# Kernel optimization log

Hardware: AMD Instinct MI355X
Metric: run time of the kernel (lower is better)

Reference implementation:

```python
import jax, jax.numpy as jnp
import numpy as np

B, H, S, D = 2, 16, 2048, 64

def setup_inputs() -> dict:
    key = jax.random.key(0)
    kq, kk, kv = jax.random.split(key, 3)
    q = jax.random.normal(kq, (B, H, S, D), dtype=jnp.float32)
    k = jax.random.normal(kk, (B, H, S, D), dtype=jnp.float32)
    v = jax.random.normal(kv, (B, H, S, D), dtype=jnp.float32)
    # causal mask: True where position j > i (future tokens are masked)
    mask = jnp.triu(jnp.ones((S, S), dtype=bool), k=1)[None, None, :, :]
    return {"q": q, "k": k, "v": v, "mask": mask}

def reference(q, k, v, mask) -> jnp.ndarray:
    # scaled dot-product attention with additive -1e4 mask bias
    scale = 1.0 / jnp.sqrt(jnp.asarray(q.shape[-1], q.dtype))
    scores = jnp.einsum('bhqd,bhkd->bhqk', q, k) * scale  # [B,H,S,S]
    scores = scores + mask.astype(scores.dtype) * jnp.asarray(-10000.0, scores.dtype)
    probs = jax.nn.softmax(scores, axis=-1)
    # dropout is identity in eval mode
    return jnp.einsum('bhqk,bhkd->bhqd', probs, v)
```

## Files before the change

kernel.cpp:

```cpp
#include <hip/hip_runtime.h>

typedef __bf16 bf16_t;
typedef bf16_t bf16x8 __attribute__((ext_vector_type(8)));
typedef bf16_t bf16x4 __attribute__((ext_vector_type(4)));
typedef float  floatx4 __attribute__((ext_vector_type(4)));

constexpr int Sq = 2048, Dq = 64;
constexpr int BQ = 64, BK = 64;
constexpr int NQT = Sq / BQ;
constexpr int STR = 72;
constexpr float SCALE_LOG2E = 0.125f * 1.44269504088896340736f;

__global__ __launch_bounds__(256, 2) void flash_attn_kernel(
    const float* __restrict__ Q, const float* __restrict__ K,
    const float* __restrict__ V, float* __restrict__ O)
{
    __shared__ bf16_t QPs[BQ][STR];
    __shared__ bf16_t Ks[BK][STR];
    __shared__ bf16_t VTs[Dq][STR];

    const int tid  = threadIdx.x;
    const int wave = tid >> 6;
    const int lane = tid & 63;
    const int quad = lane >> 4;
    const int l16  = lane & 15;

    const int id = blockIdx.x;
    const int bh = (id & 7) + ((id >> 7) << 3);
    const int pr = (id >> 3) & 15;
    const long base = (long)bh * Sq * Dq;

    const int r0 = tid >> 4;
    const int c4 = (tid & 15) * 4;
    const int h  = lane >> 3;
    const int jw = wave * 16;

    for (int half = 0; half < 2; ++half) {
        const int qt = half ? (NQT - 1 - pr) : pr;

        __syncthreads();
        #pragma unroll
        for (int p = 0; p < 4; ++p) {
            const int row = p * 16 + r0;
            const float4 qv = *(const float4*)&Q[base + (long)(qt * BQ + row) * Dq + c4];
            bf16x4 w;
            w[0] = (bf16_t)(qv.x * SCALE_LOG2E); w[1] = (bf16_t)(qv.y * SCALE_LOG2E);
            w[2] = (bf16_t)(qv.z * SCALE_LOG2E); w[3] = (bf16_t)(qv.w * SCALE_LOG2E);
            *(bf16x4*)&QPs[row][c4] = w;
        }
        __syncthreads();

        bf16x8 aq0, aq1;
        {
            const int qrow = wave * 16 + l16;
            aq0 = *(const bf16x8*)&QPs[qrow][quad * 8];
            aq1 = *(const bf16x8*)&QPs[qrow][32 + quad * 8];
        }

        float l_lane = 0.f;
        floatx4 o_acc[4];
        #pragma unroll
        for (int i = 0; i < 4; ++i) o_acc[i] = floatx4{0.f, 0.f, 0.f, 0.f};

        float4 kf[4];
        float  vf[4][4];
        #pragma unroll
        for (int p = 0; p < 4; ++p) {
            kf[p] = *(const float4*)&K[base + (long)(p * 16 + r0) * Dq + c4];
            const int j0 = jw + 4 * ((p + h) & 3);
            #pragma unroll
            for (int r = 0; r < 4; ++r)
                vf[p][r] = V[base + (long)(j0 + r) * Dq + lane];
        }

        for (int kt = 0; kt <= qt; ++kt) {
            __syncthreads();

            #pragma unroll
            for (int p = 0; p < 4; ++p) {
                bf16x4 w;
                w[0] = (bf16_t)kf[p].x; w[1] = (bf16_t)kf[p].y;
                w[2] = (bf16_t)kf[p].z; w[3] = (bf16_t)kf[p].w;
                *(bf16x4*)&Ks[p * 16 + r0][c4] = w;
                bf16x4 vw;
                vw[0] = (bf16_t)vf[p][0]; vw[1] = (bf16_t)vf[p][1];
                vw[2] = (bf16_t)vf[p][2]; vw[3] = (bf16_t)vf[p][3];
                *(bf16x4*)&VTs[lane][jw + 4 * ((p + h) & 3)] = vw;
            }
            __syncthreads();

            {
                const int kn = (kt < qt) ? (kt + 1) : qt;
                const long kb = base + (long)kn * BK * Dq;
                #pragma unroll
                for (int p = 0; p < 4; ++p) {
                    kf[p] = *(const float4*)&K[kb + (long)(p * 16 + r0) * Dq + c4];
                    const int j0 = jw + 4 * ((p + h) & 3);
                    #pragma unroll
                    for (int r = 0; r < 4; ++r)
                        vf[p][r] = V[kb + (long)(j0 + r) * Dq + lane];
                }
            }

            floatx4 acc[4];
            #pragma unroll
            for (int t = 0; t < 4; ++t) {
                acc[t] = floatx4{0.f, 0.f, 0.f, 0.f};
                const int krow = t * 16 + l16;
                bf16x8 ak0 = *(const bf16x8*)&Ks[krow][quad * 8];
                bf16x8 ak1 = *(const bf16x8*)&Ks[krow][32 + quad * 8];
                acc[t] = __builtin_amdgcn_mfma_f32_16x16x32_bf16(ak0, aq0, acc[t], 0, 0, 0);
                acc[t] = __builtin_amdgcn_mfma_f32_16x16x32_bf16(ak1, aq1, acc[t], 0, 0, 0);
            }

            if (kt == qt) {
                const int qr = wave * 16 + l16;
                #pragma unroll
                for (int t = 0; t < 4; ++t) {
                    #pragma unroll
                    for (int i = 0; i < 4; ++i) {
                        if (t * 16 + quad * 4 + i > qr) acc[t][i] = -1e30f;
                    }
                }
            }

            float l_add = 0.f;
            #pragma unroll
            for (int t = 0; t < 4; ++t) {
                #pragma unroll
                for (int i = 0; i < 4; ++i) {
                    acc[t][i] = __builtin_amdgcn_exp2f(acc[t][i]);
                    l_add += acc[t][i];
                }
            }
            l_lane += l_add;

            #pragma unroll
            for (int t = 0; t < 4; ++t) {
                bf16x4 pk;
                pk[0] = (bf16_t)acc[t][0]; pk[1] = (bf16_t)acc[t][1];
                pk[2] = (bf16_t)acc[t][2]; pk[3] = (bf16_t)acc[t][3];
                *(bf16x4*)&QPs[wave * 16 + l16][t * 16 + quad * 4] = pk;
            }

            bf16x8 ap0 = *(const bf16x8*)&QPs[wave * 16 + l16][quad * 8];
            bf16x8 ap1 = *(const bf16x8*)&QPs[wave * 16 + l16][32 + quad * 8];
            #pragma unroll
            for (int dt = 0; dt < 4; ++dt) {
                const int dcol = dt * 16 + l16;
                bf16x8 bv0 = *(const bf16x8*)&VTs[dcol][quad * 8];
                bf16x8 bv1 = *(const bf16x8*)&VTs[dcol][32 + quad * 8];
                o_acc[dt] = __builtin_amdgcn_mfma_f32_16x16x32_bf16(ap0, bv0, o_acc[dt], 0, 0, 0);
                o_acc[dt] = __builtin_amdgcn_mfma_f32_16x16x32_bf16(ap1, bv1, o_acc[dt], 0, 0, 0);
            }
        }

        float lsum = l_lane;
        lsum += __shfl_xor(lsum, 16);
        lsum += __shfl_xor(lsum, 32);
        #pragma unroll
        for (int i = 0; i < 4; ++i) {
            const float inv_l = 1.f / __shfl(lsum, quad * 4 + i, 16);
            const long row = (long)qt * BQ + wave * 16 + quad * 4 + i;
            #pragma unroll
            for (int dt = 0; dt < 4; ++dt) {
                O[base + row * Dq + dt * 16 + l16] = o_acc[dt][i] * inv_l;
            }
        }
    }
}

extern "C" void kernel_launch(void* const* d_in, const int* in_sizes, int n_in,
                              void* d_out, int out_size, void* d_ws, size_t ws_size,
                              hipStream_t stream)
{
    const float* q = (const float*)d_in[0];
    const float* k = (const float*)d_in[1];
    const float* v = (const float*)d_in[2];
    float* out = (float*)d_out;
    flash_attn_kernel<<<dim3(512, 1, 1), dim3(256, 1, 1), 0, stream>>>(q, k, v, out);
}
```

Measured before the change: 128.2 us.

## Double-buffer K/V tiles in LDS and raise wave priority around MFMAs

K and V tiles go into two LDS buffers, so the next tile is written after the PV matmul and only one barrier per iteration is needed instead of two. Global loads for the next tile are issued before the QK MFMAs. s_setprio raises wave priority during the MFMA blocks, and the exp-sum reduction is reassociated into a tree. The cost is about twice the LDS for K/V and more live registers, which may affect occupancy.

```diff
diff --git a/kernel.cpp b/kernel.cpp
--- a/kernel.cpp
+++ b/kernel.cpp
@@ -16,8 +16,8 @@
     const float* __restrict__ V, float* __restrict__ O)
 {
     __shared__ bf16_t QPs[BQ][STR];
-    __shared__ bf16_t Ks[BK][STR];
-    __shared__ bf16_t VTs[Dq][STR];
+    __shared__ bf16_t Ks[2][BK][STR];
+    __shared__ bf16_t VTs[2][Dq][STR];
 
     const int tid  = threadIdx.x;
     const int wave = tid >> 6;
@@ -62,36 +62,32 @@
         #pragma unroll
         for (int i = 0; i < 4; ++i) o_acc[i] = floatx4{0.f, 0.f, 0.f, 0.f};
 
-        float4 kf[4];
-        float  vf[4][4];
-        #pragma unroll
-        for (int p = 0; p < 4; ++p) {
-            kf[p] = *(const float4*)&K[base + (long)(p * 16 + r0) * Dq + c4];
-            const int j0 = jw + 4 * ((p + h) & 3);
+        {
             #pragma unroll
-            for (int r = 0; r < 4; ++r)
-                vf[p][r] = V[base + (long)(j0 + r) * Dq + lane];
+            for (int p = 0; p < 4; ++p) {
+                const float4 kv = *(const float4*)&K[base + (long)(p * 16 + r0) * Dq + c4];
+                bf16x4 w;
+                w[0] = (bf16_t)kv.x; w[1] = (bf16_t)kv.y;
+                w[2] = (bf16_t)kv.z; w[3] = (bf16_t)kv.w;
+                *(bf16x4*)&Ks[0][p * 16 + r0][c4] = w;
+                const int j0 = jw + 4 * ((p + h) & 3);
+                bf16x4 vw;
+                #pragma unroll
+                for (int r = 0; r < 4; ++r)
+                    vw[r] = (bf16_t)V[base + (long)(j0 + r) * Dq + lane];
+                *(bf16x4*)&VTs[0][lane][j0] = vw;
+            }
         }
+        __syncthreads();
 
         for (int kt = 0; kt <= qt; ++kt) {
-            __syncthreads();
+            const int cur  = kt & 1;
+            const bool more = (kt < qt);
 
-            #pragma unroll
-            for (int p = 0; p < 4; ++p) {
-                bf16x4 w;
-                w[0] = (bf16_t)kf[p].x; w[1] = (bf16_t)kf[p].y;
-                w[2] = (bf16_t)kf[p].z; w[3] = (bf16_t)kf[p].w;
-                *(bf16x4*)&Ks[p * 16 + r0][c4] = w;
-                bf16x4 vw;
-                vw[0] = (bf16_t)vf[p][0]; vw[1] = (bf16_t)vf[p][1];
-                vw[2] = (bf16_t)vf[p][2]; vw[3] = (bf16_t)vf[p][3];
-                *(bf16x4*)&VTs[lane][jw + 4 * ((p + h) & 3)] = vw;
-            }
-            __syncthreads();
-
-            {
-                const int kn = (kt < qt) ? (kt + 1) : qt;
-                const long kb = base + (long)kn * BK * Dq;
+            float4 kf[4];
+            float  vf[4][4];
+            if (more) {
+                const long kb = base + (long)(kt + 1) * BK * Dq;
                 #pragma unroll
                 for (int p = 0; p < 4; ++p) {
                     kf[p] = *(const float4*)&K[kb + (long)(p * 16 + r0) * Dq + c4];
@@ -103,15 +99,17 @@
             }
 
             floatx4 acc[4];
+            __builtin_amdgcn_s_setprio(1);
             #pragma unroll
             for (int t = 0; t < 4; ++t) {
                 acc[t] = floatx4{0.f, 0.f, 0.f, 0.f};
                 const int krow = t * 16 + l16;
-                bf16x8 ak0 = *(const bf16x8*)&Ks[krow][quad * 8];
-                bf16x8 ak1 = *(const bf16x8*)&Ks[krow][32 + quad * 8];
+                bf16x8 ak0 = *(const bf16x8*)&Ks[cur][krow][quad * 8];
+                bf16x8 ak1 = *(const bf16x8*)&Ks[cur][krow][32 + quad * 8];
                 acc[t] = __builtin_amdgcn_mfma_f32_16x16x32_bf16(ak0, aq0, acc[t], 0, 0, 0);
                 acc[t] = __builtin_amdgcn_mfma_f32_16x16x32_bf16(ak1, aq1, acc[t], 0, 0, 0);
             }
+            __builtin_amdgcn_s_setprio(0);
 
             if (kt == qt) {
                 const int qr = wave * 16 + l16;
@@ -124,16 +122,15 @@
                 }
             }
 
-            float l_add = 0.f;
+            float esum[4];
             #pragma unroll
             for (int t = 0; t < 4; ++t) {
                 #pragma unroll
-                for (int i = 0; i < 4; ++i) {
+                for (int i = 0; i < 4; ++i)
                     acc[t][i] = __builtin_amdgcn_exp2f(acc[t][i]);
-                    l_add += acc[t][i];
-                }
+                esum[t] = (acc[t][0] + acc[t][1]) + (acc[t][2] + acc[t][3]);
             }
-            l_lane += l_add;
+            l_lane += (esum[0] + esum[1]) + (esum[2] + esum[3]);
 
             #pragma unroll
             for (int t = 0; t < 4; ++t) {
@@ -145,13 +142,30 @@
 
             bf16x8 ap0 = *(const bf16x8*)&QPs[wave * 16 + l16][quad * 8];
             bf16x8 ap1 = *(const bf16x8*)&QPs[wave * 16 + l16][32 + quad * 8];
+            __builtin_amdgcn_s_setprio(1);
             #pragma unroll
             for (int dt = 0; dt < 4; ++dt) {
                 const int dcol = dt * 16 + l16;
-                bf16x8 bv0 = *(const bf16x8*)&VTs[dcol][quad * 8];
-                bf16x8 bv1 = *(const bf16x8*)&VTs[dcol][32 + quad * 8];
+                bf16x8 bv0 = *(const bf16x8*)&VTs[cur][dcol][quad * 8];
+                bf16x8 bv1 = *(const bf16x8*)&VTs[cur][dcol][32 + quad * 8];
                 o_acc[dt] = __builtin_amdgcn_mfma_f32_16x16x32_bf16(ap0, bv0, o_acc[dt], 0, 0, 0);
                 o_acc[dt] = __builtin_amdgcn_mfma_f32_16x16x32_bf16(ap1, bv1, o_acc[dt], 0, 0, 0);
+            }
+            __builtin_amdgcn_s_setprio(0);
+
+            if (more) {
+                #pragma unroll
+                for (int p = 0; p < 4; ++p) {
+                    bf16x4 w;
+                    w[0] = (bf16_t)kf[p].x; w[1] = (bf16_t)kf[p].y;
+                    w[2] = (bf16_t)kf[p].z; w[3] = (bf16_t)kf[p].w;
+                    *(bf16x4*)&Ks[cur ^ 1][p * 16 + r0][c4] = w;
+                    bf16x4 vw;
+                    vw[0] = (bf16_t)vf[p][0]; vw[1] = (bf16_t)vf[p][1];
+                    vw[2] = (bf16_t)vf[p][2]; vw[3] = (bf16_t)vf[p][3];
+                    *(bf16x4*)&VTs[cur ^ 1][lane][jw + 4 * ((p + h) & 3)] = vw;
+                }
+                __syncthreads();
             }
         }
 
```

After: 131.2 us. 1.02x slower.
